# Kernel tuning notes

Measured on AMD Instinct MI355X. Metric: run time of the kernel, lower is better.

## Reference

```python
import jax, jax.numpy as jnp
import numpy as np

N_VAR, N_CON, N_REG = 200_000, 100_000, 50_000
D, OUT = 128, 128
E_ADJ, E_T, E_G = 1_000_000, 500_000, 500_000
EPS = 1e-5


def setup_inputs() -> dict:
    key = jax.random.key(0)
    ks = jax.random.split(key, 16)
    s = 1.0 / np.sqrt(D)
    lin = lambda k: jax.random.uniform(k, (D, OUT), jnp.float32, -s, s)
    return {
        "x_var": jax.random.normal(ks[0], (N_VAR, D), jnp.float32),
        "x_con": jax.random.normal(ks[1], (N_CON, D), jnp.float32),
        "x_region": jax.random.normal(ks[2], (N_REG, D), jnp.float32),
        "src_adj": jax.random.randint(ks[3], (E_ADJ,), 0, N_VAR, jnp.int64 if jax.config.x64_enabled else jnp.int32),
        "dst_adj": jax.random.randint(ks[4], (E_ADJ,), 0, N_VAR, jnp.int32),
        "src_touch": jax.random.randint(ks[5], (E_T,), 0, N_VAR, jnp.int32),
        "dst_touch": jax.random.randint(ks[6], (E_T,), 0, N_CON, jnp.int32),
        "src_groups": jax.random.randint(ks[7], (E_G,), 0, N_REG, jnp.int32),
        "dst_groups": jax.random.randint(ks[8], (E_G,), 0, N_VAR, jnp.int32),
        "W_rel_adj": lin(ks[9]), "b_adj": jnp.zeros((OUT,), jnp.float32), "W_root_adj": lin(ks[10]),
        "W_rel_touch": lin(ks[11]), "b_touch": jnp.zeros((OUT,), jnp.float32), "W_root_touch": lin(ks[12]),
        "W_rel_groups": lin(ks[13]), "b_groups": jnp.zeros((OUT,), jnp.float32), "W_root_groups": lin(ks[14]),
        "gn_w_var": jnp.ones((OUT,), jnp.float32), "gn_b_var": jnp.zeros((OUT,), jnp.float32), "gn_ms_var": jnp.ones((OUT,), jnp.float32),
        "gn_w_con": jnp.ones((OUT,), jnp.float32), "gn_b_con": jnp.zeros((OUT,), jnp.float32), "gn_ms_con": jnp.ones((OUT,), jnp.float32),
    }


def _graph_conv(x_src, x_dst, src, dst, W_rel, b_rel, W_root):
    # PyG GraphConv: lin_rel(sum_{j->i} x_j) + lin_root(x_i); aggregate BEFORE linear.
    agg = jax.ops.segment_sum(x_src[src], dst, num_segments=x_dst.shape[0])
    return agg @ W_rel + b_rel + x_dst @ W_root


def _graph_norm_relu(x, w, b, mean_scale):
    # PyG GraphNorm with batch=None (single graph): per-feature stats over nodes.
    mu = jnp.mean(x, axis=0)
    xc = x - mean_scale * mu
    var = jnp.mean(xc * xc, axis=0)
    return jax.nn.relu(w * xc * jax.lax.rsqrt(var + EPS) + b)


def reference(x_var, x_con, x_region,
              src_adj, dst_adj, src_touch, dst_touch, src_groups, dst_groups,
              W_rel_adj, b_adj, W_root_adj,
              W_rel_touch, b_touch, W_root_touch,
              W_rel_groups, b_groups, W_root_groups,
              gn_w_var, gn_b_var, gn_ms_var,
              gn_w_con, gn_b_con, gn_ms_con):
    # HeteroConv(aggr='sum'): 'var' receives from 'adj' (var->var) and 'groups' (region->var)
    out_var = (_graph_conv(x_var, x_var, src_adj, dst_adj, W_rel_adj, b_adj, W_root_adj)
               + _graph_conv(x_region, x_var, src_groups, dst_groups, W_rel_groups, b_groups, W_root_groups))
    out_con = _graph_conv(x_var, x_con, src_touch, dst_touch, W_rel_touch, b_touch, W_root_touch)
    out_var = _graph_norm_relu(out_var, gn_w_var, gn_b_var, gn_ms_var)
    out_con = _graph_norm_relu(out_con, gn_w_con, gn_b_con, gn_ms_con)
    return out_var, out_con
```

## Files before the change

kernel.cpp:

```cpp
#include <hip/hip_runtime.h>
#include <hip/hip_bf16.h>

#define D 128
#define CAPB 2048
#define MAXBINS 4096

typedef __attribute__((ext_vector_type(8))) short bf16x8;
typedef __attribute__((ext_vector_type(4))) float f32x4;

__device__ __forceinline__ void atomAddF(float* p, float v) { unsafeAtomicAdd(p, v); }

__device__ __forceinline__ unsigned short f2bf(float f) {
    __hip_bfloat16 h = __float2bfloat16(f);
    return *reinterpret_cast<unsigned short*>(&h);
}
__device__ __forceinline__ float bf2f(unsigned int u16) {
    unsigned int x = u16 << 16;
    return *reinterpret_cast<float*>(&x);
}
__device__ __forceinline__ void dot2bf(float& acc, unsigned int ab, unsigned int w) {
    asm("v_dot2_f32_bf16 %0, %1, %2, %0" : "+v"(acc) : "v"(ab), "v"(w));
}

__global__ void prep_cast_zero(const float* __restrict__ Wra, const float* __restrict__ Wrg,
                               const float* __restrict__ Wrt, const float* __restrict__ Wroot_t,
                               const float* __restrict__ Wroot_a, const float* __restrict__ Wroot_g,
                               const float* __restrict__ ba, const float* __restrict__ bg,
                               unsigned short* __restrict__ Wt_adj, unsigned short* __restrict__ Wt_g,
                               unsigned short* __restrict__ Wt_t, unsigned short* __restrict__ Wt_root_t,
                               unsigned short* __restrict__ Wt_sum, float* __restrict__ bsum,
                               unsigned int* __restrict__ zbase, long zwords,
                               const float* __restrict__ xa, long n4a,
                               const float* __restrict__ xb, long n4b,
                               const float* __restrict__ xc, long n4c,
                               unsigned short* __restrict__ oa,
                               unsigned short* __restrict__ ob,
                               unsigned short* __restrict__ oc) {
    long gid = (long)blockIdx.x * blockDim.x + threadIdx.x;
    if (gid < D * D) {
        int i = (int)gid;
        int k = i >> 7, n = i & 127;
        int ti = n * D + k;
        Wt_adj[ti]    = f2bf(Wra[i]);
        Wt_g[ti]      = f2bf(Wrg[i]);
        Wt_t[ti]      = f2bf(Wrt[i]);
        Wt_root_t[ti] = f2bf(Wroot_t[i]);
        Wt_sum[ti]    = f2bf(Wroot_a[i] + Wroot_g[i]);
        if (i < D) bsum[i] = ba[i] + bg[i];
        return;
    }
    gid -= D * D;
    if (gid < zwords) { zbase[gid] = 0u; return; }
    gid -= zwords;
    const float* in; unsigned short* out; long li;
    if (gid < n4a)                 { in = xa; out = oa; li = gid; }
    else if (gid < n4a + n4b)      { in = xb; out = ob; li = gid - n4a; }
    else if (gid < n4a + n4b + n4c){ in = xc; out = oc; li = gid - n4a - n4b; }
    else return;
    float4 v = ((const float4*)in)[li];
    ushort4 o;
    o.x = f2bf(v.x); o.y = f2bf(v.y); o.z = f2bf(v.z); o.w = f2bf(v.w);
    ((ushort4*)out)[li] = o;
}

__launch_bounds__(256)
__global__ void binscatter3(const int* __restrict__ s0, const int* __restrict__ d0, int E0,
                            const int* __restrict__ s1, const int* __restrict__ d1, int E1,
                            const int* __restrict__ s2, const int* __restrict__ d2, int E2,
                            int nbV, int totBins,
                            unsigned int* __restrict__ pairs, int* __restrict__ gbincnt,
                            int* __restrict__ o0, int* __restrict__ o1, int* __restrict__ o2,
                            int* __restrict__ ovf_cnt) {
    __shared__ int lb[MAXBINS];
    const int t = threadIdx.x;
    const long Etot = (long)E0 + E1 + E2;
    const long chunk = (Etot + gridDim.x - 1) / gridDim.x;
    const long start = (long)blockIdx.x * chunk;
    long end = start + chunk; if (end > Etot) end = Etot;

    for (int b = t; b < totBins; b += 256) lb[b] = 0;
    __syncthreads();

    for (long e = start + t; e < end; e += 256) {
        int bidx;
        if (e < E0)                    bidx = (d0[e] >> 8);
        else if (e < (long)E0 + E1)    bidx = nbV + (d1[e - E0] >> 8);
        else                           bidx = 2 * nbV + (d2[e - E0 - E1] >> 8);
        atomicAdd(&lb[bidx], 1);
    }
    __syncthreads();
    for (int b = t; b < totBins; b += 256) {
        int c = lb[b];
        lb[b] = (c > 0) ? atomicAdd(&gbincnt[b], c) : 0;
    }
    __syncthreads();
    for (long e = start + t; e < end; e += 256) {
        int s, d, le, bidx; int* ovf; int* oc;
        if (e < E0)                 { le = (int)e;             s = s0[le]; d = d0[le]; bidx = (d >> 8);           ovf = o0; oc = ovf_cnt +  0; }
        else if (e < (long)E0 + E1) { le = (int)(e - E0);      s = s1[le]; d = d1[le]; bidx = nbV + (d >> 8);     ovf = o1; oc = ovf_cnt + 16; }
        else                        { le = (int)(e - E0 - E1); s = s2[le]; d = d2[le]; bidx = 2 * nbV + (d >> 8); ovf = o2; oc = ovf_cnt + 32; }
        int slot = atomicAdd(&lb[bidx], 1);
        if (slot < CAPB) pairs[(long)bidx * CAPB + slot] = ((unsigned int)s << 8) | (unsigned int)(d & 255);
        else             ovf[atomicAdd(oc, 1)] = le;
    }
}

__launch_bounds__(256)
__global__ void build_csr(int nbV, int Nvar, int Ncon,
                          const unsigned int* __restrict__ pairs, const int* __restrict__ bincnt,
                          unsigned int* __restrict__ csr, unsigned int* __restrict__ rowinfo) {
    const int b = blockIdx.x;
    int N, dstBase, infoBase;
    if (b < nbV)          { N = Nvar; dstBase = b * 256;             infoBase = 0; }
    else if (b < 2 * nbV) { N = Nvar; dstBase = (b - nbV) * 256;     infoBase = Nvar; }
    else                  { N = Ncon; dstBase = (b - 2 * nbV) * 256; infoBase = 2 * Nvar; }

    int n = bincnt[b]; if (n > CAPB) n = CAPB;
    const long base = (long)b * CAPB;
    __shared__ int hist[256], scan[256], cur[256];
    const int t = threadIdx.x;
    hist[t] = 0;
    __syncthreads();
    for (int i = t; i < n; i += 256) atomicAdd(&hist[pairs[base + i] & 255], 1);
    __syncthreads();
    scan[t] = hist[t];
    __syncthreads();
    for (int off = 1; off < 256; off <<= 1) {
        int u = (t >= off) ? scan[t - off] : 0;
        __syncthreads();
        scan[t] += u;
        __syncthreads();
    }
    const int excl = scan[t] - hist[t];
    cur[t] = excl;
    if (dstBase + t < N)
        rowinfo[infoBase + dstBase + t] = ((unsigned int)excl << 16) | (unsigned int)hist[t];
    __syncthreads();
    for (int i = t; i < n; i += 256) {
        unsigned int pr = pairs[base + i];
        int slot = atomicAdd(&cur[pr & 255], 1);
        csr[base + slot] = pr >> 8;
    }
}

__launch_bounds__(256)
__global__ void pull_csr3(int Nvar, int Ncon, int nbV,
                          const unsigned short* __restrict__ xv, const unsigned short* __restrict__ xr,
                          const unsigned int* __restrict__ csr, const unsigned int* __restrict__ rowinfo,
                          const int* __restrict__ bincnt,
                          const int* __restrict__ s0, const int* __restrict__ d0, const int* __restrict__ o0,
                          const int* __restrict__ s1, const int* __restrict__ d1, const int* __restrict__ o1,
                          const int* __restrict__ s2, const int* __restrict__ d2, const int* __restrict__ o2,
                          const int* __restrict__ ovf_cnt,
                          unsigned short* __restrict__ agg_adj, unsigned short* __restrict__ agg_g,
                          unsigned short* __restrict__ agg_t) {
    int gwid = (int)(((long)blockIdx.x * blockDim.x + threadIdx.x) >> 6);
    int lane = threadIdx.x & 63;

    const unsigned short* y; const int* src; const int* dst; const int* ovf; int oc;
    long binBase; int infoBase; int wid; unsigned short* agg;
    if (gwid < Nvar) {
        y = xv; src = s0; dst = d0; ovf = o0; oc = ovf_cnt[0];  binBase = 0;        infoBase = 0;        agg = agg_adj; wid = gwid;
    } else if (gwid < 2 * Nvar) {
        y = xr; src = s1; dst = d1; ovf = o1; oc = ovf_cnt[16]; binBase = nbV;      infoBase = Nvar;     agg = agg_g;   wid = gwid - Nvar;
    } else if (gwid < 2 * Nvar + Ncon) {
        y = xv; src = s2; dst = d2; ovf = o2; oc = ovf_cnt[32]; binBase = 2 * nbV;  infoBase = 2 * Nvar; agg = agg_t;   wid = gwid - 2 * Nvar;
    } else return;

    const int q  = lane >> 4;
    const int ql = lane & 15;
    const long colOff = (long)ql * 8;

    const unsigned int info = rowinfo[infoBase + wid];
    const int mc = (int)(info & 0xffffu);
    const long b = binBase + (wid >> 8);
    const long cbase = b * CAPB + (long)(info >> 16);

    float a0 = 0.f, a1 = 0.f, a2 = 0.f, a3 = 0.f, a4 = 0.f, a5 = 0.f, a6 = 0.f, a7 = 0.f;

    for (int cb = 0; cb < mc; cb += 64) {
        int rem = mc - cb; if (rem > 64) rem = 64;
        int idx = (lane < rem) ? (int)csr[cbase + cb + lane] : 0;
        for (int j = 0; j < rem; j += 8) {
            int e0 = j + q;
            int e1 = j + 4 + q;
            int v0 = __shfl(idx, e0, 64);
            int v1 = __shfl(idx, e1, 64);
            uint4 r0 = *(const uint4*)(y + (long)v0 * D + colOff);
            uint4 r1 = *(const uint4*)(y + (long)v1 * D + colOff);
            unsigned int w = (e0 < rem ? 0x3F80u : 0u) | (e1 < rem ? 0x3F800000u : 0u);
            unsigned int p;
            p = __builtin_amdgcn_perm(r0.x, r1.x, 0x01000504u); dot2bf(a0, p, w);
            p = __builtin_amdgcn_perm(r0.x, r1.x, 0x03020706u); dot2bf(a1, p, w);
            p = __builtin_amdgcn_perm(r0.y, r1.y, 0x01000504u); dot2bf(a2, p, w);
            p = __builtin_amdgcn_perm(r0.y, r1.y, 0x03020706u); dot2bf(a3, p, w);
            p = __builtin_amdgcn_perm(r0.z, r1.z, 0x01000504u); dot2bf(a4, p, w);
            p = __builtin_amdgcn_perm(r0.z, r1.z, 0x03020706u); dot2bf(a5, p, w);
            p = __builtin_amdgcn_perm(r0.w, r1.w, 0x01000504u); dot2bf(a6, p, w);
            p = __builtin_amdgcn_perm(r0.w, r1.w, 0x03020706u); dot2bf(a7, p, w);
        }
    }

    if (bincnt[b] > CAPB) {
        for (int i = 0; i < oc; ++i) {
            int e = ovf[i];
            if (dst[e] == wid && q == 0) {
                int s = src[e];
                uint4 r = *(const uint4*)(y + (long)s * D + colOff);
                a0 += bf2f(r.x & 0xffffu); a1 += bf2f(r.x >> 16);
                a2 += bf2f(r.y & 0xffffu); a3 += bf2f(r.y >> 16);
                a4 += bf2f(r.z & 0xffffu); a5 += bf2f(r.z >> 16);
                a6 += bf2f(r.w & 0xffffu); a7 += bf2f(r.w >> 16);
            }
        }
    }

    a0 += __shfl_xor(a0, 16, 64); a0 += __shfl_xor(a0, 32, 64);
    a1 += __shfl_xor(a1, 16, 64); a1 += __shfl_xor(a1, 32, 64);
    a2 += __shfl_xor(a2, 16, 64); a2 += __shfl_xor(a2, 32, 64);
    a3 += __shfl_xor(a3, 16, 64); a3 += __shfl_xor(a3, 32, 64);
    a4 += __shfl_xor(a4, 16, 64); a4 += __shfl_xor(a4, 32, 64);
    a5 += __shfl_xor(a5, 16, 64); a5 += __shfl_xor(a5, 32, 64);
    a6 += __shfl_xor(a6, 16, 64); a6 += __shfl_xor(a6, 32, 64);
    a7 += __shfl_xor(a7, 16, 64); a7 += __shfl_xor(a7, 32, 64);

    if (lane < 16) {
        uint4 o;
        o.x = (unsigned int)f2bf(a0) | ((unsigned int)f2bf(a1) << 16);
        o.y = (unsigned int)f2bf(a2) | ((unsigned int)f2bf(a3) << 16);
        o.z = (unsigned int)f2bf(a4) | ((unsigned int)f2bf(a5) << 16);
        o.w = (unsigned int)f2bf(a6) | ((unsigned int)f2bf(a7) << 16);
        *(uint4*)(agg + (long)wid * D + colOff) = o;
    }
}

__launch_bounds__(256, 4)
__global__ void gemm_fused(int N,
                           const unsigned short* __restrict__ A0, const unsigned short* __restrict__ Wt0,
                           const unsigned short* __restrict__ A1, const unsigned short* __restrict__ Wt1,
                           const unsigned short* __restrict__ A2, const unsigned short* __restrict__ Wt2,
                           int nTerms,
                           const float* __restrict__ bias, float* __restrict__ out,
                           float* __restrict__ gsum, float* __restrict__ gsq) {
    __shared__ unsigned short lds[2][8192];
    __shared__ float sstat[256];
    const int tx = threadIdx.x;
    sstat[tx] = 0.f;

    const int wave = tx >> 6, lane = tx & 63;
    const int quad = lane >> 4, l16 = lane & 15;
    const int row0 = blockIdx.x * 128;

    const int sA0 = tx, sA1 = tx + 256;
    const int rS0 = sA0 >> 2, qS0 = (sA0 & 3) ^ ((sA0 >> 4) & 3);
    const int rS1 = sA1 >> 2, qS1 = (sA1 & 3) ^ ((sA1 >> 4) & 3);
    long gr0 = (long)row0 + rS0; if (gr0 >= N) gr0 = N - 1;
    long gr1 = (long)row0 + rS1; if (gr1 >= N) gr1 = N - 1;

    f32x4 acc[2][8];
#pragma unroll
    for (int rt = 0; rt < 2; ++rt)
#pragma unroll
        for (int ct = 0; ct < 8; ++ct)
#pragma unroll
            for (int i = 0; i < 4; ++i) acc[rt][ct][i] = 0.f;

    auto stage = [&](int s, int bb) {
        const int t = s >> 2;
        const int k0 = (s & 3) * 32;
        const unsigned short* A = (t == 0) ? A0 : ((t == 1) ? A1 : A2);
        const unsigned short* W = (t == 0) ? Wt0 : ((t == 1) ? Wt1 : Wt2);
        __builtin_amdgcn_global_load_lds(
            (const __attribute__((address_space(1))) unsigned int*)(A + gr0 * D + k0 + qS0 * 8),
            (__attribute__((address_space(3))) unsigned int*)(&lds[bb][sA0 * 8]), 16, 0, 0);
        __builtin_amdgcn_global_load_lds(
            (const __attribute__((address_space(1))) unsigned int*)(A + gr1 * D + k0 + qS1 * 8),
            (__attribute__((address_space(3))) unsigned int*)(&lds[bb][sA1 * 8]), 16, 0, 0);
        __builtin_amdgcn_global_load_lds(
            (const __attribute__((address_space(1))) unsigned int*)(W + (long)rS0 * D + k0 + qS0 * 8),
            (__attribute__((address_space(3))) unsigned int*)(&lds[bb][4096 + sA0 * 8]), 16, 0, 0);
        __builtin_amdgcn_global_load_lds(
            (const __attribute__((address_space(1))) unsigned int*)(W + (long)rS1 * D + k0 + qS1 * 8),
            (__attribute__((address_space(3))) unsigned int*)(&lds[bb][4096 + sA1 * 8]), 16, 0, 0);
    };

    const int xq = (l16 >> 2) & 3;
    const int qx = quad ^ xq;

    auto compute = [&](int cb) {
        const int slotA0 = (wave * 32 + l16) * 4 + qx;
        const int slotA1 = (wave * 32 + 16 + l16) * 4 + qx;
        bf16x8 a0 = *(const bf16x8*)&lds[cb][slotA0 * 8];
        bf16x8 a1 = *(const bf16x8*)&lds[cb][slotA1 * 8];
#pragma unroll
        for (int ct = 0; ct < 8; ++ct) {
            const int slotB = (ct * 16 + l16) * 4 + qx;
            bf16x8 b = *(const bf16x8*)&lds[cb][4096 + slotB * 8];
            acc[0][ct] = __builtin_amdgcn_mfma_f32_16x16x32_bf16(a0, b, acc[0][ct], 0, 0, 0);
            acc[1][ct] = __builtin_amdgcn_mfma_f32_16x16x32_bf16(a1, b, acc[1][ct], 0, 0, 0);
        }
    };

    const int nsteps = nTerms * 4;
    stage(0, 0);
    __syncthreads();
    for (int s = 0; s < nsteps; ++s) {
        const int cb = s & 1;
        if (s + 1 < nsteps) stage(s + 1, cb ^ 1);
        compute(cb);
        __syncthreads();
    }

    float bv[8];
#pragma unroll
    for (int ct = 0; ct < 8; ++ct) bv[ct] = bias[ct * 16 + l16];

    float psum[8], psq[8];
#pragma unroll
    for (int ct = 0; ct < 8; ++ct) { psum[ct] = 0.f; psq[ct] = 0.f; }

#pragma unroll
    for (int rt = 0; rt < 2; ++rt)
#pragma unroll
        for (int i = 0; i < 4; ++i) {
            int row = row0 + wave * 32 + rt * 16 + quad * 4 + i;
            if (row < N) {
#pragma unroll
                for (int ct = 0; ct < 8; ++ct) {
                    float v = acc[rt][ct][i] + bv[ct];
                    out[(size_t)row * D + ct * 16 + l16] = v;
                    psum[ct] += v;
                    psq[ct] += v * v;
                }
            }
        }

#pragma unroll
    for (int ct = 0; ct < 8; ++ct) {
        atomicAdd(&sstat[ct * 16 + l16], psum[ct]);
        atomicAdd(&sstat[128 + ct * 16 + l16], psq[ct]);
    }
    __syncthreads();
    if (tx < 128) {
        atomAddF(&gsum[tx], sstat[tx]);
        atomAddF(&gsq[tx], sstat[128 + tx]);
    }
}

__global__ void norm_relu_fin(float* __restrict__ buf,
                              long nvecVar, long nvecTot,
                              const float* __restrict__ stats,
                              const float* __restrict__ wv, const float* __restrict__ bv, const float* __restrict__ msv,
                              const float* __restrict__ wc, const float* __restrict__ bc, const float* __restrict__ msc,
                              int Nvar, int Ncon) {
    __shared__ float ss[512];
    const int t = threadIdx.x;
    {
        const int col = t & 127;
        const bool isv = t < 128;
        const float n = isv ? (float)Nvar : (float)Ncon;
        const float* st = stats + (isv ? 0 : 256);
        const float mu = st[col] / n;
        const float ex2 = st[128 + col] / n;
        const float ms = (isv ? msv : msc)[col];
        const float var = ex2 - 2.f * ms * mu * mu + ms * ms * mu * mu;
        const float istd = rsqrtf(var + 1e-5f);
        const float sc = (isv ? wv : wc)[col] * istd;
        ss[(isv ? 0 : 256) + col] = sc;
        ss[(isv ? 128 : 384) + col] = (isv ? bv : bc)[col] - sc * ms * mu;
    }
    __syncthreads();
    long i = (long)blockIdx.x * blockDim.x + t;
    if (i >= nvecTot) return;
    const int base = (i < nvecVar) ? 0 : 256;
    const int q = ((int)i & 31) * 4;
    float4 v = *(float4*)(buf + i * 4);
    float4 o;
    o.x = fmaxf(0.f, v.x * ss[base + q + 0] + ss[base + 128 + q + 0]);
    o.y = fmaxf(0.f, v.y * ss[base + q + 1] + ss[base + 128 + q + 1]);
    o.z = fmaxf(0.f, v.z * ss[base + q + 2] + ss[base + 128 + q + 2]);
    o.w = fmaxf(0.f, v.w * ss[base + q + 3] + ss[base + 128 + q + 3]);
    *(float4*)(buf + i * 4) = o;
}

extern "C" void kernel_launch(void* const* d_in, const int* in_sizes, int n_in,
                              void* d_out, int out_size, void* d_ws, size_t ws_size,
                              hipStream_t stream) {
    const float* x_var = (const float*)d_in[0];
    const float* x_con = (const float*)d_in[1];
    const float* x_reg = (const float*)d_in[2];
    const int* src_adj = (const int*)d_in[3];
    const int* dst_adj = (const int*)d_in[4];
    const int* src_t   = (const int*)d_in[5];
    const int* dst_t   = (const int*)d_in[6];
    const int* src_g   = (const int*)d_in[7];
    const int* dst_g   = (const int*)d_in[8];
    const float* W_rel_adj  = (const float*)d_in[9];
    const float* b_adj      = (const float*)d_in[10];
    const float* W_root_adj = (const float*)d_in[11];
    const float* W_rel_t    = (const float*)d_in[12];
    const float* b_t        = (const float*)d_in[13];
    const float* W_root_t   = (const float*)d_in[14];
    const float* W_rel_g    = (const float*)d_in[15];
    const float* b_g        = (const float*)d_in[16];
    const float* W_root_g   = (const float*)d_in[17];
    const float* gnw_v  = (const float*)d_in[18];
    const float* gnb_v  = (const float*)d_in[19];
    const float* gnms_v = (const float*)d_in[20];
    const float* gnw_c  = (const float*)d_in[21];
    const float* gnb_c  = (const float*)d_in[22];
    const float* gnms_c = (const float*)d_in[23];

    const int Nvar = in_sizes[0] / D;
    const int Ncon = in_sizes[1] / D;
    const int Nreg = in_sizes[2] / D;
    const int Eadj = in_sizes[3];
    const int Et   = in_sizes[5];
    const int Eg   = in_sizes[7];

    const int nbV = (Nvar + 255) >> 8;
    const int nbC = (Ncon + 255) >> 8;
    const int totBins = 2 * nbV + nbC;

    char* p = (char*)d_ws;
    unsigned short* xv_bf = (unsigned short*)p; p += (size_t)Nvar * D * 2;
    unsigned short* xc_bf = (unsigned short*)p; p += (size_t)Ncon * D * 2;
    unsigned short* xr_bf = (unsigned short*)p; p += (size_t)Nreg * D * 2;
    unsigned short* agg_adj = (unsigned short*)p; p += (size_t)Nvar * D * 2;
    unsigned short* agg_g   = (unsigned short*)p; p += (size_t)Nvar * D * 2;
    unsigned short* agg_t   = (unsigned short*)p; p += (size_t)Ncon * D * 2;
    unsigned int* pairs = (unsigned int*)p; p += (size_t)totBins * CAPB * 4;
    unsigned int* csr   = (unsigned int*)p; p += (size_t)totBins * CAPB * 4;
    unsigned int* rowinfo = (unsigned int*)p; p += (size_t)(2 * Nvar + Ncon) * 4;
    int* ovf0 = (int*)p; p += (size_t)Eadj * 4;
    int* ovf1 = (int*)p; p += (size_t)Eg * 4;
    int* ovf2 = (int*)p; p += (size_t)Et * 4;
    unsigned short* Wt_adj    = (unsigned short*)p; p += D * D * 2;
    unsigned short* Wt_g      = (unsigned short*)p; p += D * D * 2;
    unsigned short* Wt_t      = (unsigned short*)p; p += D * D * 2;
    unsigned short* Wt_root_t = (unsigned short*)p; p += D * D * 2;
    unsigned short* Wt_sum    = (unsigned short*)p; p += D * D * 2;
    float* bsum  = (float*)p; p += D * 4;
    char* zbase = p;
    float* stats   = (float*)p; p += 512 * 4;
    int* ovf_cnt   = (int*)p;   p += 64 * 4;
    int* bincnt    = (int*)p;   p += (size_t)totBins * 4;
    const long zwords = (long)(p - zbase) / 4;

    float* out_var = (float*)d_out;
    float* out_con = out_var + (size_t)Nvar * D;

    {
        long n4v = (long)Nvar * 32, n4c = (long)Ncon * 32, n4r = (long)Nreg * 32;
        long tot = (long)D * D + zwords + n4v + n4c + n4r;
        prep_cast_zero<<<(int)((tot + 255) / 256), 256, 0, stream>>>(
            W_rel_adj, W_rel_g, W_rel_t, W_root_t, W_root_adj, W_root_g, b_adj, b_g,
            Wt_adj, Wt_g, Wt_t, Wt_root_t, Wt_sum, bsum,
            (unsigned int*)zbase, zwords,
            x_var, n4v, x_con, n4c, x_reg, n4r, xv_bf, xc_bf, xr_bf);
    }

    binscatter3<<<128, 256, 0, stream>>>(
        src_adj, dst_adj, Eadj,
        src_g,   dst_g,   Eg,
        src_t,   dst_t,   Et,
        nbV, totBins, pairs, bincnt, ovf0, ovf1, ovf2, ovf_cnt);

    build_csr<<<totBins, 256, 0, stream>>>(nbV, Nvar, Ncon, pairs, bincnt, csr, rowinfo);

    {
        long T = ((long)2 * Nvar + Ncon) * 64;
        pull_csr3<<<(int)((T + 255) / 256), 256, 0, stream>>>(
            Nvar, Ncon, nbV, xv_bf, xr_bf,
            csr, rowinfo, bincnt,
            src_adj, dst_adj, ovf0,
            src_g,   dst_g,   ovf1,
            src_t,   dst_t,   ovf2,
            ovf_cnt, agg_adj, agg_g, agg_t);
    }

    gemm_fused<<<(Nvar + 127) / 128, 256, 0, stream>>>(Nvar,
        agg_adj, Wt_adj, agg_g, Wt_g, xv_bf, Wt_sum, 3,
        bsum, out_var, stats, stats + 128);
    gemm_fused<<<(Ncon + 127) / 128, 256, 0, stream>>>(Ncon,
        agg_t, Wt_t, xc_bf, Wt_root_t, nullptr, nullptr, 2,
        b_t, out_con, stats + 256, stats + 384);

    {
        long nvecVar = (long)Nvar * 32;
        long nvecTot = (long)(Nvar + Ncon) * 32;
        norm_relu_fin<<<(int)((nvecTot + 255) / 256), 256, 0, stream>>>(
            out_var, nvecVar, nvecTot, stats,
            gnw_v, gnb_v, gnms_v, gnw_c, gnb_c, gnms_c, Nvar, Ncon);
    }
}
```

Before: 754.7 us.

## Assign one row per 16-lane quarter-wave in CSR pull aggregation

The pull-aggregation kernel now maps four destination rows to each wave, one per 16-lane group, instead of one row per full wave. That removes the cross-quarter shuffle reduction and launches a quarter as many waves. Each group loads 4 neighbor rows per step for more memory-level parallelism, and bf16 packing uses a single cvt_pk instruction. The risk is divergence, since each wave now loops until its longest row finishes, and the per-row edge counts vary.

```diff
diff --git a/kernel.cpp b/kernel.cpp
--- a/kernel.cpp
+++ b/kernel.cpp
@@ -20,6 +20,11 @@
 }
 __device__ __forceinline__ void dot2bf(float& acc, unsigned int ab, unsigned int w) {
     asm("v_dot2_f32_bf16 %0, %1, %2, %0" : "+v"(acc) : "v"(ab), "v"(w));
+}
+__device__ __forceinline__ unsigned int pk_bf16(float lo, float hi) {
+    unsigned int r;
+    asm("v_cvt_pk_bf16_f32 %0, %1, %2" : "=v"(r) : "v"(lo), "v"(hi));
+    return r;
 }
 
 __global__ void prep_cast_zero(const float* __restrict__ Wra, const float* __restrict__ Wrg,
@@ -154,82 +159,92 @@
                           const int* __restrict__ ovf_cnt,
                           unsigned short* __restrict__ agg_adj, unsigned short* __restrict__ agg_g,
                           unsigned short* __restrict__ agg_t) {
-    int gwid = (int)(((long)blockIdx.x * blockDim.x + threadIdx.x) >> 6);
-    int lane = threadIdx.x & 63;
-
-    const unsigned short* y; const int* src; const int* dst; const int* ovf; int oc;
-    long binBase; int infoBase; int wid; unsigned short* agg;
-    if (gwid < Nvar) {
-        y = xv; src = s0; dst = d0; ovf = o0; oc = ovf_cnt[0];  binBase = 0;        infoBase = 0;        agg = agg_adj; wid = gwid;
-    } else if (gwid < 2 * Nvar) {
-        y = xr; src = s1; dst = d1; ovf = o1; oc = ovf_cnt[16]; binBase = nbV;      infoBase = Nvar;     agg = agg_g;   wid = gwid - Nvar;
-    } else if (gwid < 2 * Nvar + Ncon) {
-        y = xv; src = s2; dst = d2; ovf = o2; oc = ovf_cnt[32]; binBase = 2 * nbV;  infoBase = 2 * Nvar; agg = agg_t;   wid = gwid - 2 * Nvar;
-    } else return;
-
-    const int q  = lane >> 4;
+    const int tx = threadIdx.x;
+    const int lane = tx & 63;
     const int ql = lane & 15;
+    const int sl = lane & 48;
     const long colOff = (long)ql * 8;
 
+    const long tot = 2L * Nvar + Ncon;
+    const long wv = ((long)blockIdx.x * blockDim.x + tx) >> 6;
+    long r = wv * 4 + (lane >> 4);
+    const bool active = r < tot;
+    if (!active) r = tot - 1;
+
+    const bool g1 = (r >= Nvar) && (r < 2L * Nvar);
+    const bool g2 = (r >= 2L * Nvar);
+    const unsigned short* y = g1 ? xr : xv;
+    const int wid = (int)(r - (g1 ? (long)Nvar : 0) - (g2 ? 2L * Nvar : 0));
+    const int infoBase = g1 ? Nvar : (g2 ? 2 * Nvar : 0);
+    const long binBase = g1 ? nbV : (g2 ? 2L * nbV : 0);
+    unsigned short* agg = g1 ? agg_g : (g2 ? agg_t : agg_adj);
+
     const unsigned int info = rowinfo[infoBase + wid];
-    const int mc = (int)(info & 0xffffu);
+    const int mc = active ? (int)(info & 0xffffu) : 0;
     const long b = binBase + (wid >> 8);
     const long cbase = b * CAPB + (long)(info >> 16);
 
     float a0 = 0.f, a1 = 0.f, a2 = 0.f, a3 = 0.f, a4 = 0.f, a5 = 0.f, a6 = 0.f, a7 = 0.f;
 
-    for (int cb = 0; cb < mc; cb += 64) {
-        int rem = mc - cb; if (rem > 64) rem = 64;
-        int idx = (lane < rem) ? (int)csr[cbase + cb + lane] : 0;
-        for (int j = 0; j < rem; j += 8) {
-            int e0 = j + q;
-            int e1 = j + 4 + q;
-            int v0 = __shfl(idx, e0, 64);
-            int v1 = __shfl(idx, e1, 64);
-            uint4 r0 = *(const uint4*)(y + (long)v0 * D + colOff);
-            uint4 r1 = *(const uint4*)(y + (long)v1 * D + colOff);
-            unsigned int w = (e0 < rem ? 0x3F80u : 0u) | (e1 < rem ? 0x3F800000u : 0u);
+    for (int base = 0; __any(base < mc); base += 16) {
+        int idx = (base + ql < mc) ? (int)csr[cbase + base + ql] : 0;
+        for (int jj = 0; jj < 16; jj += 4) {
+            const int e = base + jj;
+            if (!__any(e < mc)) break;
+            int i0 = __shfl(idx, sl + jj + 0, 64);
+            int i1 = __shfl(idx, sl + jj + 1, 64);
+            int i2 = __shfl(idx, sl + jj + 2, 64);
+            int i3 = __shfl(idx, sl + jj + 3, 64);
+            uint4 r0 = *(const uint4*)(y + (long)i0 * D + colOff);
+            uint4 r1 = *(const uint4*)(y + (long)i1 * D + colOff);
+            uint4 r2 = *(const uint4*)(y + (long)i2 * D + colOff);
+            uint4 r3 = *(const uint4*)(y + (long)i3 * D + colOff);
+            unsigned int w01 = ((e     < mc) ? 0x3F80u : 0u) | ((e + 1 < mc) ? 0x3F800000u : 0u);
+            unsigned int w23 = ((e + 2 < mc) ? 0x3F80u : 0u) | ((e + 3 < mc) ? 0x3F800000u : 0u);
             unsigned int p;
-            p = __builtin_amdgcn_perm(r0.x, r1.x, 0x01000504u); dot2bf(a0, p, w);
-            p = __builtin_amdgcn_perm(r0.x, r1.x, 0x03020706u); dot2bf(a1, p, w);
-            p = __builtin_amdgcn_perm(r0.y, r1.y, 0x01000504u); dot2bf(a2, p, w);
-            p = __builtin_amdgcn_perm(r0.y, r1.y, 0x03020706u); dot2bf(a3, p, w);
-            p = __builtin_amdgcn_perm(r0.z, r1.z, 0x01000504u); dot2bf(a4, p, w);
-            p = __builtin_amdgcn_perm(r0.z, r1.z, 0x03020706u); dot2bf(a5, p, w);
-            p = __builtin_amdgcn_perm(r0.w, r1.w, 0x01000504u); dot2bf(a6, p, w);
-            p = __builtin_amdgcn_perm(r0.w, r1.w, 0x03020706u); dot2bf(a7, p, w);
+            p = __builtin_amdgcn_perm(r0.x, r1.x, 0x01000504u); dot2bf(a0, p, w01);
+            p = __builtin_amdgcn_perm(r2.x, r3.x, 0x01000504u); dot2bf(a0, p, w23);
+            p = __builtin_amdgcn_perm(r0.x, r1.x, 0x03020706u); dot2bf(a1, p, w01);
+            p = __builtin_amdgcn_perm(r2.x, r3.x, 0x03020706u); dot2bf(a1, p, w23);
+            p = __builtin_amdgcn_perm(r0.y, r1.y, 0x01000504u); dot2bf(a2, p, w01);
+            p = __builtin_amdgcn_perm(r2.y, r3.y, 0x01000504u); dot2bf(a2, p, w23);
+            p = __builtin_amdgcn_perm(r0.y, r1.y, 0x03020706u); dot2bf(a3, p, w01);
+            p = __builtin_amdgcn_perm(r2.y, r3.y, 0x03020706u); dot2bf(a3, p, w23);
+            p = __builtin_amdgcn_perm(r0.z, r1.z, 0x01000504u); dot2bf(a4, p, w01);
+            p = __builtin_amdgcn_perm(r2.z, r3.z, 0x01000504u); dot2bf(a4, p, w23);
+            p = __builtin_amdgcn_perm(r0.z, r1.z, 0x03020706u); dot2bf(a5, p, w01);
+            p = __builtin_amdgcn_perm(r2.z, r3.z, 0x03020706u); dot2bf(a5, p, w23);
+            p = __builtin_amdgcn_perm(r0.w, r1.w, 0x01000504u); dot2bf(a6, p, w01);
+            p = __builtin_amdgcn_perm(r2.w, r3.w, 0x01000504u); dot2bf(a6, p, w23);
+            p = __builtin_amdgcn_perm(r0.w, r1.w, 0x03020706u); dot2bf(a7, p, w01);
+            p = __builtin_amdgcn_perm(r2.w, r3.w, 0x03020706u); dot2bf(a7, p, w23);
         }
     }
 
-    if (bincnt[b] > CAPB) {
+    if (active && bincnt[b] > CAPB) {
+        const int* srcp = g1 ? s1 : (g2 ? s2 : s0);
+        const int* dstp = g1 ? d1 : (g2 ? d2 : d0);
+        const int* ovf  = g1 ? o1 : (g2 ? o2 : o0);
+        const int oc = ovf_cnt[g1 ? 16 : (g2 ? 32 : 0)];
         for (int i = 0; i < oc; ++i) {
             int e = ovf[i];
-            if (dst[e] == wid && q == 0) {
-                int s = src[e];
-                uint4 r = *(const uint4*)(y + (long)s * D + colOff);
-                a0 += bf2f(r.x & 0xffffu); a1 += bf2f(r.x >> 16);
-                a2 += bf2f(r.y & 0xffffu); a3 += bf2f(r.y >> 16);
-                a4 += bf2f(r.z & 0xffffu); a5 += bf2f(r.z >> 16);
-                a6 += bf2f(r.w & 0xffffu); a7 += bf2f(r.w >> 16);
+            if (dstp[e] == wid) {
+                int s = srcp[e];
+                uint4 rr = *(const uint4*)(y + (long)s * D + colOff);
+                a0 += bf2f(rr.x & 0xffffu); a1 += bf2f(rr.x >> 16);
+                a2 += bf2f(rr.y & 0xffffu); a3 += bf2f(rr.y >> 16);
+                a4 += bf2f(rr.z & 0xffffu); a5 += bf2f(rr.z >> 16);
+                a6 += bf2f(rr.w & 0xffffu); a7 += bf2f(rr.w >> 16);
             }
         }
     }
 
-    a0 += __shfl_xor(a0, 16, 64); a0 += __shfl_xor(a0, 32, 64);
-    a1 += __shfl_xor(a1, 16, 64); a1 += __shfl_xor(a1, 32, 64);
-    a2 += __shfl_xor(a2, 16, 64); a2 += __shfl_xor(a2, 32, 64);
-    a3 += __shfl_xor(a3, 16, 64); a3 += __shfl_xor(a3, 32, 64);
-    a4 += __shfl_xor(a4, 16, 64); a4 += __shfl_xor(a4, 32, 64);
-    a5 += __shfl_xor(a5, 16, 64); a5 += __shfl_xor(a5, 32, 64);
-    a6 += __shfl_xor(a6, 16, 64); a6 += __shfl_xor(a6, 32, 64);
-    a7 += __shfl_xor(a7, 16, 64); a7 += __shfl_xor(a7, 32, 64);
-
-    if (lane < 16) {
+    if (active) {
         uint4 o;
-        o.x = (unsigned int)f2bf(a0) | ((unsigned int)f2bf(a1) << 16);
-        o.y = (unsigned int)f2bf(a2) | ((unsigned int)f2bf(a3) << 16);
-        o.z = (unsigned int)f2bf(a4) | ((unsigned int)f2bf(a5) << 16);
-        o.w = (unsigned int)f2bf(a6) | ((unsigned int)f2bf(a7) << 16);
+        o.x = pk_bf16(a0, a1);
+        o.y = pk_bf16(a2, a3);
+        o.z = pk_bf16(a4, a5);
+        o.w = pk_bf16(a6, a7);
         *(uint4*)(agg + (long)wid * D + colOff) = o;
     }
 }
@@ -469,7 +484,8 @@
     build_csr<<<totBins, 256, 0, stream>>>(nbV, Nvar, Ncon, pairs, bincnt, csr, rowinfo);
 
     {
-        long T = ((long)2 * Nvar + Ncon) * 64;
+        long rows = (long)2 * Nvar + Ncon;
+        long T = ((rows + 3) / 4) * 64;
         pull_csr3<<<(int)((T + 255) / 256), 256, 0, stream>>>(
             Nvar, Ncon, nbV, xv_bf, xr_bf,
             csr, rowinfo, bincnt,
```

Result: faster. 680.3 us (-9.9%).
